# Optimization experiments

Hardware: AMD Instinct MI355X
Metric: run time of the kernel (lower is better)

## Reference

```python
import jax, jax.numpy as jnp
import numpy as np

N = 100000      # nodes
E = 1600000     # edges (avg degree 16)
DIN = 128
DOUT = 128


def setup_inputs() -> dict:
    key = jax.random.key(0)
    k1, k2, k3, k4 = jax.random.split(key, 4)
    x = jax.random.normal(k1, (N, DIN), dtype=jnp.float32)
    edge_index = jax.random.randint(k2, (2, E), 0, N, dtype=jnp.int64)
    # guarantee every node appears at least once as a source row so that
    # degree > 0 everywhere (1/sqrt(0) would be inf, as in the torch code)
    row = edge_index[0].at[:N].set(jnp.arange(N, dtype=jnp.int64))
    edge_index = jnp.stack([row, edge_index[1]])
    W = jax.random.normal(k3, (DOUT, DIN), dtype=jnp.float32) / np.sqrt(DIN)
    b = jax.random.normal(k4, (DOUT,), dtype=jnp.float32) * 0.01
    return {"x": x, "edge_index": edge_index, "W": W, "b": b}


def reference(x, edge_index, W, b):
    # Math identical to: A = dense(add_self_loops(edge_index));
    # D = 1/sqrt(degree(edge_index[0]))  (degree WITHOUT self-loops);
    # out = (D_i * A_ij * D_j) @ (x W^T + b)
    row, col = edge_index[0], edge_index[1]
    deg = jax.ops.segment_sum(jnp.ones(row.shape[0], x.dtype), row, num_segments=N)
    d = jax.lax.rsqrt(deg)                      # [N]
    h = x @ W.T + b                             # [N, DOUT]
    # edge contributions: out[r] += D[r] * D[c] * h[c]  (duplicate edges sum, as to_dense does)
    agg = jax.ops.segment_sum(d[col][:, None] * h[col], row, num_segments=N)
    # self-loop term added for every node: D[i]^2 * h[i]
    out = d[:, None] * agg + (d * d)[:, None] * h
    return out
```

## Files before the change

kernel.cpp:

```cpp
#include <hip/hip_runtime.h>

#define D 128
#define BROWS 1024
#define CAP 17408
#define CHUNK 2048

typedef __attribute__((ext_vector_type(8))) short bf16x8;
typedef __attribute__((ext_vector_type(4))) float f32x4;

__device__ inline unsigned short f2bf(float f) {
    unsigned u = __float_as_uint(f);
    u += 0x7FFFu + ((u >> 16) & 1u);
    return (unsigned short)(u >> 16);
}
__device__ inline float bf2f(unsigned short h) {
    return __uint_as_float((unsigned)h << 16);
}
__device__ inline float bflo(unsigned u) { return __uint_as_float(u << 16); }
__device__ inline float bfhi(unsigned u) { return __uint_as_float(u & 0xFFFF0000u); }

__global__ __launch_bounds__(256) void k_bin(const int* __restrict__ row,
                                             const int* __restrict__ col,
                                             int E, int* __restrict__ gcur,
                                             unsigned* __restrict__ ebuf) {
    __shared__ int lhist[128];
    __shared__ int sc[128];
    __shared__ int gbase[128];
    __shared__ unsigned sstage[CHUNK];
    __shared__ int sdest[CHUNK];
    int t = threadIdx.x;
    int base = blockIdx.x * CHUNK;
    if (t < 128) lhist[t] = 0;
    __syncthreads();
    int b[8], p[8]; unsigned pk[8];
    #pragma unroll
    for (int i = 0; i < 8; ++i) {
        int idx = base + i * 256 + t;
        if (idx < E) {
            int r = row[idx], c = col[idx];
            b[i] = r >> 10;
            pk[i] = ((unsigned)(r & (BROWS - 1)) << 17) | (unsigned)c;
            p[i] = atomicAdd(&lhist[b[i]], 1);
        } else b[i] = -1;
    }
    __syncthreads();
    if (t < 64) {
        int a0 = lhist[2 * t], a1 = lhist[2 * t + 1];
        int s = a0 + a1;
        int incl = s;
        #pragma unroll
        for (int m = 1; m < 64; m <<= 1) {
            int tmp = __shfl_up(incl, m);
            if (t >= m) incl += tmp;
        }
        int excl = incl - s;
        sc[2 * t] = excl;
        sc[2 * t + 1] = excl + a0;
        if (a0 > 0) gbase[2 * t] = atomicAdd(&gcur[2 * t], a0);
        if (a1 > 0) gbase[2 * t + 1] = atomicAdd(&gcur[2 * t + 1], a1);
    }
    __syncthreads();
    #pragma unroll
    for (int i = 0; i < 8; ++i) {
        if (b[i] >= 0) {
            int lidx = sc[b[i]] + p[i];
            int rel = gbase[b[i]] + p[i];
            sstage[lidx] = pk[i];
            sdest[lidx] = (rel < CAP) ? (b[i] * CAP + rel) : -1;
        }
    }
    __syncthreads();
    int total = sc[127] + lhist[127];
    for (int i = t; i < total; i += 256) {
        int d = sdest[i];
        if (d >= 0) ebuf[d] = sstage[i];
    }
}

__global__ __launch_bounds__(1024) void k_group(const int* __restrict__ gcur,
                                                const unsigned* __restrict__ ebuf,
                                                int N, int NBK,
                                                float* __restrict__ dvals,
                                                int* __restrict__ rptr,
                                                int* __restrict__ csr_col) {
    __shared__ unsigned sebuf[CAP];
    __shared__ int lhist[1024];
    __shared__ int wtot[16];
    __shared__ int woff[16];
    __shared__ int sebase;
    int bkt = blockIdx.x, t = threadIdx.x;
    int cnt = gcur[bkt]; if (cnt > CAP) cnt = CAP;
    if (t < 64) {
        int acc = 0;
        for (int i = t; i < bkt; i += 64) {
            int g = gcur[i];
            acc += (g > CAP) ? CAP : g;
        }
        #pragma unroll
        for (int m = 1; m < 64; m <<= 1) acc += __shfl_xor(acc, m);
        if (t == 0) sebase = acc;
    }
    lhist[t] = 0;
    __syncthreads();
    const unsigned* ep = ebuf + (size_t)bkt * CAP;
    for (int i = t; i < cnt; i += 1024) {
        unsigned e = ep[i];
        sebuf[i] = e;
        atomicAdd(&lhist[e >> 17], 1);
    }
    __syncthreads();
    int v = lhist[t];
    int lane = t & 63, wv = t >> 6;
    int incl = v;
    #pragma unroll
    for (int m = 1; m < 64; m <<= 1) {
        int tmp = __shfl_up(incl, m);
        if (lane >= m) incl += tmp;
    }
    if (lane == 63) wtot[wv] = incl;
    __syncthreads();
    if (t < 16) {
        int w = wtot[t];
        int wincl = w;
        #pragma unroll
        for (int m = 1; m < 16; m <<= 1) {
            int tmp = __shfl_up(wincl, m);
            if (t >= m) wincl += tmp;
        }
        woff[t] = wincl - w;
    }
    __syncthreads();
    int excl = woff[wv] + incl - v;
    int ebase = sebase;
    int r = (bkt << 10) + t;
    if (r < N) {
        rptr[r] = ebase + excl;
        dvals[r] = rsqrtf((float)v);
    }
    if (bkt == NBK - 1 && t == 0) rptr[N] = ebase + cnt;
    lhist[t] = excl;
    __syncthreads();
    for (int i = t; i < cnt; i += 1024) {
        unsigned e = sebuf[i];
        int rr = (int)(e >> 17);
        int p = atomicAdd(&lhist[rr], 1);
        csr_col[ebase + p] = (int)(e & 0x1FFFFu);
    }
}

__global__ void k_cast(const float* __restrict__ x, const float* __restrict__ dvals,
                       unsigned short* __restrict__ xs, int total4) {
    int i = blockIdx.x * blockDim.x + threadIdx.x;
    if (i >= total4) return;
    float4 v = ((const float4*)x)[i];
    float d = dvals[i >> 5];
    ushort4 o = make_ushort4(f2bf(d * v.x), f2bf(d * v.y), f2bf(d * v.z), f2bf(d * v.w));
    ((ushort4*)xs)[i] = o;
}

#define ACC8(v) do { \
    a[0] += bflo((v).x); a[1] += bfhi((v).x); \
    a[2] += bflo((v).y); a[3] += bfhi((v).y); \
    a[4] += bflo((v).z); a[5] += bfhi((v).z); \
    a[6] += bflo((v).w); a[7] += bfhi((v).w); } while (0)

__global__ __launch_bounds__(256) void k_rows(const unsigned short* __restrict__ xs,
                                              const int* __restrict__ rptr,
                                              const int* __restrict__ csr_col,
                                              const float* __restrict__ dvals,
                                              float* __restrict__ ssum,
                                              float* __restrict__ y, int N) {
    int wid = (blockIdx.x * blockDim.x + threadIdx.x) >> 6;
    if (wid >= N) return;
    int lane = threadIdx.x & 63;
    int grp = lane >> 4, sl = lane & 15;
    int s = rptr[wid];
    int n = rptr[wid + 1] - s;
    const uint4* xsv = (const uint4*)xs;

    int ccreg = (lane < n) ? csr_col[s + lane] : 0;
    float sd = (lane < n) ? dvals[ccreg] : 0.f;
    uint4 vself = make_uint4(0, 0, 0, 0);
    if (grp == 0) vself = xsv[wid * 16 + sl];

    float a[8] = {0.f, 0.f, 0.f, 0.f, 0.f, 0.f, 0.f, 0.f};
    int nf = (n < 64) ? n : 64;
    for (int k0 = 0; k0 < nf; k0 += 16) {
        int i0 = k0 + grp, i1 = i0 + 4, i2 = i0 + 8, i3 = i0 + 12;
        int cc0 = __shfl(ccreg, i0), cc1 = __shfl(ccreg, i1);
        int cc2 = __shfl(ccreg, i2), cc3 = __shfl(ccreg, i3);
        bool p0 = i0 < nf, p1 = i1 < nf, p2 = i2 < nf, p3 = i3 < nf;
        uint4 v0, v1, v2, v3;
        if (p0) v0 = xsv[cc0 * 16 + sl];
        if (p1) v1 = xsv[cc1 * 16 + sl];
        if (p2) v2 = xsv[cc2 * 16 + sl];
        if (p3) v3 = xsv[cc3 * 16 + sl];
        if (p0) ACC8(v0);
        if (p1) ACC8(v1);
        if (p2) ACC8(v2);
        if (p3) ACC8(v3);
    }
    if (__builtin_expect(n > 64, 0)) {
        for (int idx = 64 + grp; idx < n; idx += 4) {
            int cc = csr_col[s + idx];
            uint4 v = xsv[cc * 16 + sl];
            ACC8(v);
        }
        for (int idx = 64 + lane; idx < n; idx += 64)
            sd += dvals[csr_col[s + idx]];
    }
    if (grp == 0) ACC8(vself);

    #pragma unroll
    for (int j = 0; j < 8; ++j) {
        a[j] += __shfl_xor(a[j], 16);
        a[j] += __shfl_xor(a[j], 32);
    }
    #pragma unroll
    for (int m = 1; m < 64; m <<= 1) sd += __shfl_xor(sd, m);

    float dr = dvals[wid];
    if (grp < 2) {
        float4 o = (grp == 0) ? make_float4(a[0], a[1], a[2], a[3])
                              : make_float4(a[4], a[5], a[6], a[7]);
        o.x *= dr; o.y *= dr; o.z *= dr; o.w *= dr;
        ((float4*)(y + (size_t)wid * D))[sl * 2 + grp] = o;
    }
    if (lane == 0) ssum[wid] = dr * (dr + sd);
}

#define LDSW 136

__global__ __launch_bounds__(256, 2) void k_gemm(const float* __restrict__ W,
                                                 const float* __restrict__ b,
                                                 const float* __restrict__ ssum,
                                                 float* yo, int N) {
    __shared__ unsigned short Whi[128 * LDSW];
    __shared__ unsigned short Wlo[128 * LDSW];
    __shared__ float bs[D];
    int t = threadIdx.x;
    #pragma unroll
    for (int i = 0; i < 16; ++i) {
        int idx4 = i * 256 + t;
        float4 w4 = ((const float4*)W)[idx4];
        int r = idx4 >> 5;
        int c = (idx4 & 31) * 4;
        unsigned short h0 = f2bf(w4.x), h1 = f2bf(w4.y), h2 = f2bf(w4.z), h3 = f2bf(w4.w);
        unsigned short l0 = f2bf(w4.x - bf2f(h0));
        unsigned short l1 = f2bf(w4.y - bf2f(h1));
        unsigned short l2 = f2bf(w4.z - bf2f(h2));
        unsigned short l3 = f2bf(w4.w - bf2f(h3));
        ushort4* ph = (ushort4*)&Whi[r * LDSW + c];
        ushort4* pl = (ushort4*)&Wlo[r * LDSW + c];
        *ph = make_ushort4(h0, h1, h2, h3);
        *pl = make_ushort4(l0, l1, l2, l3);
    }
    if (t < D) bs[t] = b[t];
    __syncthreads();

    int wave = t >> 6, lane = t & 63;
    int quad = lane >> 4, mrow = lane & 15;
    int row_base = blockIdx.x * 128 + wave * 32;

    bf16x8 Ahi[2][4], Alo[2][4];
    #pragma unroll
    for (int s = 0; s < 2; ++s) {
        int grow = row_base + s * 16 + mrow;
        bool ok = grow < N;
        const float* yrow = yo + (size_t)(ok ? grow : 0) * D;
        #pragma unroll
        for (int kk = 0; kk < 4; ++kk) {
            int k0 = kk * 32 + quad * 8;
            float4 f0 = ok ? ((const float4*)(yrow + k0))[0] : make_float4(0, 0, 0, 0);
            float4 f1 = ok ? ((const float4*)(yrow + k0))[1] : make_float4(0, 0, 0, 0);
            float fv[8] = {f0.x, f0.y, f0.z, f0.w, f1.x, f1.y, f1.z, f1.w};
            #pragma unroll
            for (int j = 0; j < 8; ++j) {
                unsigned short h = f2bf(fv[j]);
                Ahi[s][kk][j] = (short)h;
                Alo[s][kk][j] = (short)f2bf(fv[j] - bf2f(h));
            }
        }
    }

    f32x4 acc[2][8];
    #pragma unroll
    for (int s = 0; s < 2; ++s)
        #pragma unroll
        for (int ct = 0; ct < 8; ++ct)
            acc[s][ct] = (f32x4){0.f, 0.f, 0.f, 0.f};

    #pragma unroll
    for (int ct = 0; ct < 8; ++ct) {
        int wrow = ct * 16 + mrow;
        #pragma unroll
        for (int kk = 0; kk < 4; ++kk) {
            int off = wrow * LDSW + kk * 32 + quad * 8;
            bf16x8 Bhi = *(const bf16x8*)&Whi[off];
            bf16x8 Blo = *(const bf16x8*)&Wlo[off];
            #pragma unroll
            for (int s = 0; s < 2; ++s) {
                acc[s][ct] = __builtin_amdgcn_mfma_f32_16x16x32_bf16(Ahi[s][kk], Bhi, acc[s][ct], 0, 0, 0);
                acc[s][ct] = __builtin_amdgcn_mfma_f32_16x16x32_bf16(Alo[s][kk], Bhi, acc[s][ct], 0, 0, 0);
                acc[s][ct] = __builtin_amdgcn_mfma_f32_16x16x32_bf16(Ahi[s][kk], Blo, acc[s][ct], 0, 0, 0);
            }
        }
    }

    #pragma unroll
    for (int s = 0; s < 2; ++s) {
        #pragma unroll
        for (int r = 0; r < 4; ++r) {
            int grow = row_base + s * 16 + quad * 4 + r;
            if (grow < N) {
                float sv = ssum[grow];
                #pragma unroll
                for (int ct = 0; ct < 8; ++ct) {
                    int col = ct * 16 + mrow;
                    yo[(size_t)grow * D + col] = acc[s][ct][r] + sv * bs[col];
                }
            }
        }
    }
}

extern "C" void kernel_launch(void* const* d_in, const int* in_sizes, int n_in,
                              void* d_out, int out_size, void* d_ws, size_t ws_size,
                              hipStream_t stream) {
    const float* x  = (const float*)d_in[0];
    const int*   ei = (const int*)d_in[1];
    const float* W  = (const float*)d_in[2];
    const float* b  = (const float*)d_in[3];
    float* out = (float*)d_out;
    int N = in_sizes[0] / D;
    int E = in_sizes[1] / 2;
    int NBK = (N + BROWS - 1) / BROWS;
    int NCH = (E + CHUNK - 1) / CHUNK;

    int*      gcur    = (int*)d_ws;
    int*      rptr    = gcur + 128;
    float*    dvals   = (float*)(rptr + N + 1);
    float*    ssum    = dvals + N;
    int*      csr_col = (int*)(ssum + N);
    unsigned* ebuf    = (unsigned*)(csr_col + E);
    uintptr_t xs_addr = (uintptr_t)(ebuf + (size_t)NBK * CAP);
    xs_addr = (xs_addr + 15) & ~(uintptr_t)15;
    unsigned short* xs = (unsigned short*)xs_addr;

    hipMemsetAsync(gcur, 0, 128 * sizeof(int), stream);
    k_bin<<<NCH, 256, 0, stream>>>(ei, ei + E, E, gcur, ebuf);
    k_group<<<NBK, 1024, 0, stream>>>(gcur, ebuf, N, NBK, dvals, rptr, csr_col);
    k_cast<<<(N * (D / 4) + 255) / 256, 256, 0, stream>>>(x, dvals, xs, N * (D / 4));
    k_rows<<<(N + 3) / 4, 256, 0, stream>>>(xs, rptr, csr_col, dvals, ssum, out, N);
    k_gemm<<<(N + 127) / 128, 256, 0, stream>>>(W, b, ssum, out, N);
}
```

Before: 276.6 us.

## Fuse cast into group kernel, shrink buckets, precompute W splits, unroll gather

Halves the bucket size to 512 rows, giving 196 buckets instead of 98 for better GPU occupancy. Each k_bin block now handles a larger chunk with 512 threads, and the first blocks precompute the bf16 hi/lo split of W once instead of every GEMM block redoing it. The separate cast kernel is fused into k_group, so each bucket scales and casts its own x rows, saving one launch and a dvals reload. The gather loop is unrolled to 8 unpredicated loads per lane, using sentinel zero rows and a zero degree entry, to raise memory-level parallelism at the cost of wasted loads for low-degree rows.

After: 276.8 us. About the same (+0.1%).

```diff
diff --git a/kernel.cpp b/kernel.cpp
--- a/kernel.cpp
+++ b/kernel.cpp
@@ -1,9 +1,11 @@
 #include <hip/hip_runtime.h>
 
 #define D 128
-#define BROWS 1024
-#define CAP 17408
-#define CHUNK 2048
+#define BROWS 512
+#define LOGB 9
+#define NBMAX 256
+#define CAP 9216
+#define CHUNK 4096
 
 typedef __attribute__((ext_vector_type(8))) short bf16x8;
 typedef __attribute__((ext_vector_type(4))) float f32x4;
@@ -19,34 +21,48 @@
 __device__ inline float bflo(unsigned u) { return __uint_as_float(u << 16); }
 __device__ inline float bfhi(unsigned u) { return __uint_as_float(u & 0xFFFF0000u); }
 
-__global__ __launch_bounds__(256) void k_bin(const int* __restrict__ row,
+__global__ __launch_bounds__(512) void k_bin(const int* __restrict__ row,
                                              const int* __restrict__ col,
                                              int E, int* __restrict__ gcur,
-                                             unsigned* __restrict__ ebuf) {
-    __shared__ int lhist[128];
-    __shared__ int sc[128];
-    __shared__ int gbase[128];
+                                             unsigned* __restrict__ ebuf,
+                                             const float* __restrict__ W,
+                                             unsigned short* __restrict__ Wbh,
+                                             unsigned short* __restrict__ Wbl) {
+    __shared__ int lhist[NBMAX];
+    __shared__ int sc[NBMAX];
+    __shared__ int gbase[NBMAX];
     __shared__ unsigned sstage[CHUNK];
     __shared__ int sdest[CHUNK];
     int t = threadIdx.x;
+    if (blockIdx.x < 8) {
+        int base = blockIdx.x * 2048 + t;
+        #pragma unroll
+        for (int i = 0; i < 4; ++i) {
+            int idx = base + i * 512;
+            float wv = W[idx];
+            unsigned short h = f2bf(wv);
+            Wbh[idx] = h;
+            Wbl[idx] = f2bf(wv - bf2f(h));
+        }
+    }
     int base = blockIdx.x * CHUNK;
-    if (t < 128) lhist[t] = 0;
+    if (t < NBMAX) lhist[t] = 0;
     __syncthreads();
     int b[8], p[8]; unsigned pk[8];
     #pragma unroll
     for (int i = 0; i < 8; ++i) {
-        int idx = base + i * 256 + t;
+        int idx = base + i * 512 + t;
         if (idx < E) {
             int r = row[idx], c = col[idx];
-            b[i] = r >> 10;
+            b[i] = r >> LOGB;
             pk[i] = ((unsigned)(r & (BROWS - 1)) << 17) | (unsigned)c;
             p[i] = atomicAdd(&lhist[b[i]], 1);
         } else b[i] = -1;
     }
     __syncthreads();
     if (t < 64) {
-        int a0 = lhist[2 * t], a1 = lhist[2 * t + 1];
-        int s = a0 + a1;
+        int a0 = lhist[4*t], a1 = lhist[4*t+1], a2 = lhist[4*t+2], a3 = lhist[4*t+3];
+        int s = a0 + a1 + a2 + a3;
         int incl = s;
         #pragma unroll
         for (int m = 1; m < 64; m <<= 1) {
@@ -54,10 +70,12 @@
             if (t >= m) incl += tmp;
         }
         int excl = incl - s;
-        sc[2 * t] = excl;
-        sc[2 * t + 1] = excl + a0;
-        if (a0 > 0) gbase[2 * t] = atomicAdd(&gcur[2 * t], a0);
-        if (a1 > 0) gbase[2 * t + 1] = atomicAdd(&gcur[2 * t + 1], a1);
+        sc[4*t] = excl; sc[4*t+1] = excl + a0;
+        sc[4*t+2] = excl + a0 + a1; sc[4*t+3] = excl + a0 + a1 + a2;
+        if (a0 > 0) gbase[4*t]   = atomicAdd(&gcur[4*t],   a0);
+        if (a1 > 0) gbase[4*t+1] = atomicAdd(&gcur[4*t+1], a1);
+        if (a2 > 0) gbase[4*t+2] = atomicAdd(&gcur[4*t+2], a2);
+        if (a3 > 0) gbase[4*t+3] = atomicAdd(&gcur[4*t+3], a3);
     }
     __syncthreads();
     #pragma unroll
@@ -70,8 +88,8 @@
         }
     }
     __syncthreads();
-    int total = sc[127] + lhist[127];
-    for (int i = t; i < total; i += 256) {
+    int total = sc[NBMAX - 1] + lhist[NBMAX - 1];
+    for (int i = t; i < total; i += 512) {
         int d = sdest[i];
         if (d >= 0) ebuf[d] = sstage[i];
     }
@@ -79,14 +97,17 @@
 
 __global__ __launch_bounds__(1024) void k_group(const int* __restrict__ gcur,
                                                 const unsigned* __restrict__ ebuf,
+                                                const float* __restrict__ x,
                                                 int N, int NBK,
                                                 float* __restrict__ dvals,
                                                 int* __restrict__ rptr,
-                                                int* __restrict__ csr_col) {
+                                                int* __restrict__ csr_col,
+                                                unsigned short* __restrict__ xs) {
     __shared__ unsigned sebuf[CAP];
-    __shared__ int lhist[1024];
-    __shared__ int wtot[16];
-    __shared__ int woff[16];
+    __shared__ int lhist[BROWS];
+    __shared__ float sdl[BROWS];
+    __shared__ int wtot[8];
+    __shared__ int woff[8];
     __shared__ int sebase;
     int bkt = blockIdx.x, t = threadIdx.x;
     int cnt = gcur[bkt]; if (cnt > CAP) cnt = CAP;
@@ -100,7 +121,7 @@
         for (int m = 1; m < 64; m <<= 1) acc += __shfl_xor(acc, m);
         if (t == 0) sebase = acc;
     }
-    lhist[t] = 0;
+    if (t < BROWS) lhist[t] = 0;
     __syncthreads();
     const unsigned* ep = ebuf + (size_t)bkt * CAP;
     for (int i = t; i < cnt; i += 1024) {
@@ -109,36 +130,44 @@
         atomicAdd(&lhist[e >> 17], 1);
     }
     __syncthreads();
-    int v = lhist[t];
     int lane = t & 63, wv = t >> 6;
-    int incl = v;
-    #pragma unroll
-    for (int m = 1; m < 64; m <<= 1) {
-        int tmp = __shfl_up(incl, m);
-        if (lane >= m) incl += tmp;
-    }
-    if (lane == 63) wtot[wv] = incl;
-    __syncthreads();
-    if (t < 16) {
+    int v = 0, incl = 0;
+    if (t < BROWS) {
+        v = lhist[t];
+        incl = v;
+        #pragma unroll
+        for (int m = 1; m < 64; m <<= 1) {
+            int tmp = __shfl_up(incl, m);
+            if (lane >= m) incl += tmp;
+        }
+        if (lane == 63) wtot[wv] = incl;
+    }
+    __syncthreads();
+    if (t < 8) {
         int w = wtot[t];
         int wincl = w;
         #pragma unroll
-        for (int m = 1; m < 16; m <<= 1) {
+        for (int m = 1; m < 8; m <<= 1) {
             int tmp = __shfl_up(wincl, m);
             if (t >= m) wincl += tmp;
         }
         woff[t] = wincl - w;
     }
     __syncthreads();
-    int excl = woff[wv] + incl - v;
     int ebase = sebase;
-    int r = (bkt << 10) + t;
-    if (r < N) {
-        rptr[r] = ebase + excl;
-        dvals[r] = rsqrtf((float)v);
+    if (t < BROWS) {
+        int excl = woff[wv] + incl - v;
+        int r = (bkt << LOGB) + t;
+        float dl = rsqrtf((float)v);
+        if (r < N) {
+            rptr[r] = ebase + excl;
+            dvals[r] = dl;
+        }
+        sdl[t] = dl;
+        lhist[t] = excl;
     }
     if (bkt == NBK - 1 && t == 0) rptr[N] = ebase + cnt;
-    lhist[t] = excl;
+    if (bkt == 0 && t == 0) dvals[N] = 0.f;
     __syncthreads();
     for (int i = t; i < cnt; i += 1024) {
         unsigned e = sebuf[i];
@@ -146,16 +175,21 @@
         int p = atomicAdd(&lhist[rr], 1);
         csr_col[ebase + p] = (int)(e & 0x1FFFFu);
     }
-}
-
-__global__ void k_cast(const float* __restrict__ x, const float* __restrict__ dvals,
-                       unsigned short* __restrict__ xs, int total4) {
-    int i = blockIdx.x * blockDim.x + threadIdx.x;
-    if (i >= total4) return;
-    float4 v = ((const float4*)x)[i];
-    float d = dvals[i >> 5];
-    ushort4 o = make_ushort4(f2bf(d * v.x), f2bf(d * v.y), f2bf(d * v.z), f2bf(d * v.w));
-    ((ushort4*)xs)[i] = o;
+    int rb = bkt << LOGB;
+    const float4* x4 = (const float4*)x;
+    for (int idx = t; idx < BROWS * 32; idx += 1024) {
+        int rl = idx >> 5;
+        int r = rb + rl;
+        if (r < N) {
+            float4 vv = x4[(size_t)r * 32 + (idx & 31)];
+            float d = sdl[rl];
+            ushort4 o = make_ushort4(f2bf(d * vv.x), f2bf(d * vv.y),
+                                     f2bf(d * vv.z), f2bf(d * vv.w));
+            ((ushort4*)xs)[(size_t)r * 32 + (idx & 31)] = o;
+        }
+    }
+    if (bkt == 0 && t < 64)
+        ((unsigned*)(xs + (size_t)N * D))[t] = 0u;
 }
 
 #define ACC8(v) do { \
@@ -178,32 +212,35 @@
     int n = rptr[wid + 1] - s;
     const uint4* xsv = (const uint4*)xs;
 
-    int ccreg = (lane < n) ? csr_col[s + lane] : 0;
-    float sd = (lane < n) ? dvals[ccreg] : 0.f;
-    uint4 vself = make_uint4(0, 0, 0, 0);
-    if (grp == 0) vself = xsv[wid * 16 + sl];
+    int cc0 = csr_col[s + lane];
+    int ccreg = (lane < n) ? cc0 : N;
+    float sd = dvals[ccreg];
+    uint4 vself = xsv[(size_t)wid * 16 + sl];
 
     float a[8] = {0.f, 0.f, 0.f, 0.f, 0.f, 0.f, 0.f, 0.f};
     int nf = (n < 64) ? n : 64;
-    for (int k0 = 0; k0 < nf; k0 += 16) {
-        int i0 = k0 + grp, i1 = i0 + 4, i2 = i0 + 8, i3 = i0 + 12;
-        int cc0 = __shfl(ccreg, i0), cc1 = __shfl(ccreg, i1);
-        int cc2 = __shfl(ccreg, i2), cc3 = __shfl(ccreg, i3);
-        bool p0 = i0 < nf, p1 = i1 < nf, p2 = i2 < nf, p3 = i3 < nf;
-        uint4 v0, v1, v2, v3;
-        if (p0) v0 = xsv[cc0 * 16 + sl];
-        if (p1) v1 = xsv[cc1 * 16 + sl];
-        if (p2) v2 = xsv[cc2 * 16 + sl];
-        if (p3) v3 = xsv[cc3 * 16 + sl];
-        if (p0) ACC8(v0);
-        if (p1) ACC8(v1);
-        if (p2) ACC8(v2);
-        if (p3) ACC8(v3);
+    for (int k0 = 0; k0 < nf; k0 += 32) {
+        int i0 = k0 + grp;
+        int c0 = __shfl(ccreg, i0),      c1 = __shfl(ccreg, i0 + 4);
+        int c2 = __shfl(ccreg, i0 + 8),  c3 = __shfl(ccreg, i0 + 12);
+        int c4 = __shfl(ccreg, i0 + 16), c5 = __shfl(ccreg, i0 + 20);
+        int c6 = __shfl(ccreg, i0 + 24), c7 = __shfl(ccreg, i0 + 28);
+        uint4 v0 = xsv[(size_t)c0 * 16 + sl];
+        uint4 v1 = xsv[(size_t)c1 * 16 + sl];
+        uint4 v2 = xsv[(size_t)c2 * 16 + sl];
+        uint4 v3 = xsv[(size_t)c3 * 16 + sl];
+        uint4 v4 = xsv[(size_t)c4 * 16 + sl];
+        uint4 v5 = xsv[(size_t)c5 * 16 + sl];
+        uint4 v6 = xsv[(size_t)c6 * 16 + sl];
+        uint4 v7 = xsv[(size_t)c7 * 16 + sl];
+        __builtin_amdgcn_sched_barrier(0);
+        ACC8(v0); ACC8(v1); ACC8(v2); ACC8(v3);
+        ACC8(v4); ACC8(v5); ACC8(v6); ACC8(v7);
     }
     if (__builtin_expect(n > 64, 0)) {
         for (int idx = 64 + grp; idx < n; idx += 4) {
             int cc = csr_col[s + idx];
-            uint4 v = xsv[cc * 16 + sl];
+            uint4 v = xsv[(size_t)cc * 16 + sl];
             ACC8(v);
         }
         for (int idx = 64 + lane; idx < n; idx += 64)
@@ -231,7 +268,8 @@
 
 #define LDSW 136
 
-__global__ __launch_bounds__(256, 2) void k_gemm(const float* __restrict__ W,
+__global__ __launch_bounds__(256, 2) void k_gemm(const unsigned short* __restrict__ Wbh,
+                                                 const unsigned short* __restrict__ Wbl,
                                                  const float* __restrict__ b,
                                                  const float* __restrict__ ssum,
                                                  float* yo, int N) {
@@ -242,18 +280,10 @@
     #pragma unroll
     for (int i = 0; i < 16; ++i) {
         int idx4 = i * 256 + t;
-        float4 w4 = ((const float4*)W)[idx4];
         int r = idx4 >> 5;
         int c = (idx4 & 31) * 4;
-        unsigned short h0 = f2bf(w4.x), h1 = f2bf(w4.y), h2 = f2bf(w4.z), h3 = f2bf(w4.w);
-        unsigned short l0 = f2bf(w4.x - bf2f(h0));
-        unsigned short l1 = f2bf(w4.y - bf2f(h1));
-        unsigned short l2 = f2bf(w4.z - bf2f(h2));
-        unsigned short l3 = f2bf(w4.w - bf2f(h3));
-        ushort4* ph = (ushort4*)&Whi[r * LDSW + c];
-        ushort4* pl = (ushort4*)&Wlo[r * LDSW + c];
-        *ph = make_ushort4(h0, h1, h2, h3);
-        *pl = make_ushort4(l0, l1, l2, l3);
+        ((ushort4*)&Whi[r * LDSW + c])[0] = ((const ushort4*)Wbh)[idx4];
+        ((ushort4*)&Wlo[r * LDSW + c])[0] = ((const ushort4*)Wbl)[idx4];
     }
     if (t < D) bs[t] = b[t];
     __syncthreads();
@@ -334,23 +364,24 @@
     float* out = (float*)d_out;
     int N = in_sizes[0] / D;
     int E = in_sizes[1] / 2;
-    int NBK = (N + BROWS - 1) / BROWS;
+    int NB = (N + BROWS - 1) / BROWS;
     int NCH = (E + CHUNK - 1) / CHUNK;
 
-    int*      gcur    = (int*)d_ws;
-    int*      rptr    = gcur + 128;
-    float*    dvals   = (float*)(rptr + N + 1);
-    float*    ssum    = dvals + N;
-    int*      csr_col = (int*)(ssum + N);
-    unsigned* ebuf    = (unsigned*)(csr_col + E);
-    uintptr_t xs_addr = (uintptr_t)(ebuf + (size_t)NBK * CAP);
+    int*            gcur    = (int*)d_ws;
+    int*            rptr    = gcur + NBMAX;
+    float*          dvals   = (float*)(rptr + N + 1);
+    float*          ssum    = dvals + N + 1;
+    int*            csr_col = (int*)(ssum + N);
+    unsigned*       ebuf    = (unsigned*)(csr_col + E + 64);
+    unsigned short* Wbh     = (unsigned short*)(ebuf + (size_t)NB * CAP);
+    unsigned short* Wbl     = Wbh + D * D;
+    uintptr_t xs_addr = (uintptr_t)(Wbl + D * D);
     xs_addr = (xs_addr + 15) & ~(uintptr_t)15;
     unsigned short* xs = (unsigned short*)xs_addr;
 
-    hipMemsetAsync(gcur, 0, 128 * sizeof(int), stream);
-    k_bin<<<NCH, 256, 0, stream>>>(ei, ei + E, E, gcur, ebuf);
-    k_group<<<NBK, 1024, 0, stream>>>(gcur, ebuf, N, NBK, dvals, rptr, csr_col);
-    k_cast<<<(N * (D / 4) + 255) / 256, 256, 0, stream>>>(x, dvals, xs, N * (D / 4));
+    hipMemsetAsync(gcur, 0, NBMAX * sizeof(int), stream);
+    k_bin<<<NCH, 512, 0, stream>>>(ei, ei + E, E, gcur, ebuf, W, Wbh, Wbl);
+    k_group<<<NB, 1024, 0, stream>>>(gcur, ebuf, x, N, NB, dvals, rptr, csr_col, xs);
     k_rows<<<(N + 3) / 4, 256, 0, stream>>>(xs, rptr, csr_col, dvals, ssum, out, N);
-    k_gemm<<<(N + 127) / 128, 256, 0, stream>>>(W, b, ssum, out, N);
-}
+    k_gemm<<<(N + 127) / 128, 256, 0, stream>>>(Wbh, Wbl, b, ssum, out, N);
+}
```
